# Performance work log

Hardware: AMD Instinct MI355X
Metric: run time of the kernel (lower is better)

Reference implementation:

```python
import jax, jax.numpy as jnp
import numpy as np

N = 50000    # total nodes in a batched graph
E = 200000   # directed edges (before self loops)
G = 256      # molecules per batch
F_IN = 64    # atom features
H = 4        # gat heads
CH = 128     # hidden_channels (per head)
D = H * CH   # 512, concat width
MLP_H = 128  # hidden_channels * mlp_hidden_factor
NEG_SLOPE = 0.2


def _gat(x, src, dst, W, a_src, a_dst, b, concat):
    """PyG GATConv (eval mode, self loops already added to src/dst)."""
    n = x.shape[0]
    heads, ch = a_src.shape
    h = (x @ W).reshape(n, heads, ch)                       # [N,H,C]
    e = jax.nn.leaky_relu((h * a_src).sum(-1)[src]
                          + (h * a_dst).sum(-1)[dst], NEG_SLOPE)  # [E,H]
    emax = jax.ops.segment_max(e, dst, num_segments=n)
    emax = jnp.where(jnp.isfinite(emax), emax, 0.0)
    p = jnp.exp(e - emax[dst])
    denom = jax.ops.segment_sum(p, dst, num_segments=n)
    alpha = p / (denom[dst] + 1e-16)                        # segment softmax over dst
    out = jax.ops.segment_sum(h[src] * alpha[..., None], dst, num_segments=n)
    out = out.reshape(n, heads * ch) if concat else out.mean(axis=1)
    return out + b


def _encoder(x, edge_index, batch, p):
    n = x.shape[0]
    loop = jnp.arange(n, dtype=edge_index.dtype)            # GATConv add_self_loops=True
    src = jnp.concatenate([edge_index[0], loop])
    dst = jnp.concatenate([edge_index[1], loop])
    x = jax.nn.elu(_gat(x, src, dst, p['W1'], p['as1'], p['ad1'], p['b1'], True))
    x = jax.nn.elu(_gat(x, src, dst, p['W2'], p['as2'], p['ad2'], p['b2'], True))
    x = _gat(x, src, dst, p['W3'], p['as3'], p['ad3'], p['b3'], False)
    emb = jax.ops.segment_max(x, batch, num_segments=G)     # global_max_pool
    return jnp.where(jnp.isfinite(emb), emb, 0.0)


def setup_inputs() -> dict:
    key = jax.random.key(0)
    ks = jax.random.split(key, 24)
    rn = lambda k, s, sc=0.1: jax.random.normal(k, s, jnp.float32) * sc
    return dict(
        x1=rn(ks[0], (N, F_IN), 1.0),
        edge_index1=jax.random.randint(ks[1], (2, E), 0, N, dtype=jnp.int32),
        batch1=jnp.sort(jax.random.randint(ks[2], (N,), 0, G, dtype=jnp.int32)),
        x2=rn(ks[3], (N, F_IN), 1.0),
        edge_index2=jax.random.randint(ks[4], (2, E), 0, N, dtype=jnp.int32),
        batch2=jnp.sort(jax.random.randint(ks[5], (N,), 0, G, dtype=jnp.int32)),
        W1=rn(ks[6], (F_IN, D)), as1=rn(ks[7], (H, CH)), ad1=rn(ks[8], (H, CH)),
        b1=jnp.zeros((D,), jnp.float32),
        W2=rn(ks[9], (D, D)), as2=rn(ks[10], (H, CH)), ad2=rn(ks[11], (H, CH)),
        b2=jnp.zeros((D,), jnp.float32),
        W3=rn(ks[12], (D, CH)), as3=rn(ks[13], (1, CH)), ad3=rn(ks[14], (1, CH)),
        b3=jnp.zeros((CH,), jnp.float32),
        mw1=rn(ks[15], (2 * CH, MLP_H)), mb1=jnp.zeros((MLP_H,), jnp.float32),
        mw2=rn(ks[16], (MLP_H, 1)), mb2=jnp.zeros((1,), jnp.float32),
    )


def reference(x1, edge_index1, batch1, x2, edge_index2, batch2,
              W1, as1, ad1, b1, W2, as2, ad2, b2, W3, as3, ad3, b3,
              mw1, mb1, mw2, mb2):
    p = dict(W1=W1, as1=as1, ad1=ad1, b1=b1,
             W2=W2, as2=as2, ad2=ad2, b2=b2,
             W3=W3, as3=as3, ad3=ad3, b3=b3)
    e1 = _encoder(x1, edge_index1, batch1, p)               # [G, CH]
    e2 = _encoder(x2, edge_index2, batch2, p)               # [G, CH]
    z = jnp.concatenate([e1, e2], axis=-1)                  # [G, 2*CH]
    return jax.nn.relu(z @ mw1 + mb1) @ mw2 + mb2           # [G, 1]
```

## Files before the change

### kernel.cpp

```cpp
#include <hip/hip_runtime.h>
#include <cstdint>

namespace {
constexpr int kN = 50000;
constexpr int kE = 200000;
constexpr int kE2 = kE + kN;
constexpr int kG = 256;
constexpr float kNegSlope = 0.2f;
}

using half8   = __attribute__((ext_vector_type(8))) _Float16;
using half2v  = __attribute__((ext_vector_type(2))) _Float16;
using floatx4 = __attribute__((ext_vector_type(4))) float;

__device__ __forceinline__ void gld_lds16(const void* g, void* l) {
  __builtin_amdgcn_global_load_lds(
      (const __attribute__((address_space(1))) unsigned int*)g,
      (__attribute__((address_space(3))) unsigned int*)l, 16, 0, 0);
}

__device__ __forceinline__ float fexp(float x) {
  return __builtin_amdgcn_exp2f(x * 1.44269504088896f);
}

template <int OUTF16, int BN, int CT>
__global__ __launch_bounds__(256, 2) void gemm_ring(
    const _Float16* __restrict__ A, const _Float16* __restrict__ B,
    void* __restrict__ Cv, int M, int N, int K) {
  constexpr int ASL = 512;
  constexpr int BSL = BN * 4;
  constexpr int SLOT = (ASL + BSL) * 16;
  constexpr int LPT = (ASL + BSL) / 256;
  constexpr int WTM = 64;
  constexpr int WTN = BN / 2;
  constexpr int MI = WTM / 16;
  constexpr int NI = WTN / 16;
  __shared__ alignas(16) char smem[3 * SLOT];
  const int t = threadIdx.x;
  const int w = t >> 6, l = t & 63;
  const int x = blockIdx.x & 7, s = blockIdx.x >> 3;
  const int col = (CT == 1) ? 0 : (s & (CT - 1));
  const int rt = ((CT == 1) ? s : (s >> 1)) * 8 + x;
  const int bm = rt * 128;
  const int bn = col * BN;
  if (bm >= M) return;
  const int wr = w >> 1, wc = w & 1;
  const int quad = l >> 4, lrow = l & 15;

  floatx4 acc[MI][NI];
#pragma unroll
  for (int mi = 0; mi < MI; ++mi)
#pragma unroll
    for (int ni = 0; ni < NI; ++ni) acc[mi][ni] = (floatx4){0.f, 0.f, 0.f, 0.f};

  auto stageA = [&](int slot, int kt) {
    char* buf = smem + (size_t)slot * SLOT;
    int k0 = kt * 32;
    k0 = (k0 > K - 32) ? (K - 32) : k0;
#pragma unroll
    for (int i = 0; i < ASL / 256; ++i) {
      const int sl = i * 256 + t;
      const int row = ((sl >> 6) << 4) + (sl & 15);
      const int q = (sl >> 4) & 3;
      int ga = bm + row;
      ga = (ga < M) ? ga : (M - 1);
      gld_lds16(A + (size_t)ga * K + k0 + q * 8, buf + sl * 16);
    }
  };
  auto stageB = [&](int slot, int kt) {
    char* buf = smem + (size_t)slot * SLOT + ASL * 16;
    int k0 = kt * 32;
    k0 = (k0 > K - 32) ? (K - 32) : k0;
#pragma unroll
    for (int i = 0; i < BSL / 256; ++i) {
      const int sl = i * 256 + t;
      const int row = ((sl >> 6) << 4) + (sl & 15);
      const int q = (sl >> 4) & 3;
      gld_lds16(B + (size_t)(bn + row) * K + k0 + q * 8, buf + sl * 16);
    }
  };

  stageA(0, 0); stageB(0, 0);
  stageA(1, 1); stageB(1, 1);

  const int NT = K >> 5;
  int cur = 0;
  for (int kt = 0; kt < NT; ++kt) {
    char* bufc = smem + (size_t)cur * SLOT;
    const int stg = (cur == 0) ? 2 : (cur - 1);
    if constexpr (LPT == 6)
      asm volatile("s_waitcnt vmcnt(6)" ::: "memory");
    else
      asm volatile("s_waitcnt vmcnt(4)" ::: "memory");
    __builtin_amdgcn_s_barrier();
    asm volatile("" ::: "memory");
    stageA(stg, kt + 2);
    half8 fa[MI], fb[NI];
#pragma unroll
    for (int ni = 0; ni < NI; ++ni)
      fb[ni] = *(const half8*)(bufc + ASL * 16 + ((wc * NI + ni) << 10) + l * 16);
#pragma unroll
    for (int mi = 0; mi < MI / 2; ++mi)
      fa[mi] = *(const half8*)(bufc + ((wr * MI + mi) << 10) + l * 16);
    __builtin_amdgcn_s_setprio(1);
#pragma unroll
    for (int mi = 0; mi < MI / 2; ++mi)
#pragma unroll
      for (int ni = 0; ni < NI; ++ni)
        acc[mi][ni] = __builtin_amdgcn_mfma_f32_16x16x32_f16(
            fa[mi], fb[ni], acc[mi][ni], 0, 0, 0);
    __builtin_amdgcn_s_setprio(0);
    stageB(stg, kt + 2);
#pragma unroll
    for (int mi = MI / 2; mi < MI; ++mi)
      fa[mi] = *(const half8*)(bufc + ((wr * MI + mi) << 10) + l * 16);
    __builtin_amdgcn_s_setprio(1);
#pragma unroll
    for (int mi = MI / 2; mi < MI; ++mi)
#pragma unroll
      for (int ni = 0; ni < NI; ++ni)
        acc[mi][ni] = __builtin_amdgcn_mfma_f32_16x16x32_f16(
            fa[mi], fb[ni], acc[mi][ni], 0, 0, 0);
    __builtin_amdgcn_s_setprio(0);
    cur = (cur == 2) ? 0 : (cur + 1);
  }
  asm volatile("s_waitcnt vmcnt(0)" ::: "memory");
  const int colbase = bn + wc * WTN + lrow;
#pragma unroll
  for (int mi = 0; mi < MI; ++mi) {
    const int rbase = bm + wr * WTM + mi * 16 + quad * 4;
#pragma unroll
    for (int r = 0; r < 4; ++r) {
      const int grow = rbase + r;
      if (grow < M) {
        if constexpr (OUTF16) {
          _Float16* C = (_Float16*)Cv;
#pragma unroll
          for (int ni = 0; ni < NI; ++ni)
            C[(size_t)grow * N + colbase + ni * 16] = (_Float16)acc[mi][ni][r];
        } else {
          float* C = (float*)Cv;
#pragma unroll
          for (int ni = 0; ni < NI; ++ni)
            C[(size_t)grow * N + colbase + ni * 16] = acc[mi][ni][r];
        }
      }
    }
  }
}

__global__ void wt_split_all(const float* __restrict__ W1, _Float16* Th1,
                             const float* __restrict__ W2, _Float16* Th2,
                             const float* __restrict__ W3, _Float16* Th3) {
  int idx = blockIdx.x * blockDim.x + threadIdx.x;
  const float* W;
  _Float16* Th;
  int K, N;
  if (idx < 64 * 512) {
    W = W1; Th = Th1; K = 64; N = 512;
  } else if (idx < 64 * 512 + 512 * 512) {
    idx -= 64 * 512;
    W = W2; Th = Th2; K = 512; N = 512;
  } else if (idx < 64 * 512 + 512 * 512 + 512 * 128) {
    idx -= 64 * 512 + 512 * 512;
    W = W3; Th = Th3; K = 512; N = 128;
  } else {
    return;
  }
  const int k = idx / N;
  const int n = idx - k * N;
  Th[n * K + k] = (_Float16)W[idx];
}

__global__ void prep_all(const float* __restrict__ x0, const float* __restrict__ x1,
                         _Float16* __restrict__ Xh, int* __restrict__ cnt,
                         int* __restrict__ total,
                         const float* __restrict__ W1, _Float16* Th1,
                         const float* __restrict__ W2, _Float16* Th2,
                         const float* __restrict__ W3, _Float16* Th3) {
  const int idx = blockIdx.x * blockDim.x + threadIdx.x;
  const int half = kN * 64;
  if (idx < half) {
    Xh[idx] = (_Float16)x0[idx];
  } else if (idx < 2 * half) {
    Xh[idx] = (_Float16)x1[idx - half];
  } else {
    int e = idx - 2 * half;
    const float* W;
    _Float16* Th;
    int K, N;
    if (e < 64 * 512) {
      W = W1; Th = Th1; K = 64; N = 512;
    } else if (e < 64 * 512 + 512 * 512) {
      e -= 64 * 512;
      W = W2; Th = Th2; K = 512; N = 512;
    } else if (e < 64 * 512 + 512 * 512 + 512 * 128) {
      e -= 64 * 512 + 512 * 512;
      W = W3; Th = Th3; K = 512; N = 128;
    } else {
      W = nullptr; Th = nullptr; K = N = 0;
    }
    if (W) {
      const int k = e / N;
      const int n = e - k * N;
      Th[n * K + k] = (_Float16)W[e];
    }
  }
  if (idx < 2 * kN) cnt[idx] = 1;
  if (idx == 0) *total = 0;
}
__global__ void prep(const float* __restrict__ X, _Float16* __restrict__ Xh,
                     int* __restrict__ cnt, int* __restrict__ total, int nsplit,
                     int n) {
  const int idx = blockIdx.x * blockDim.x + threadIdx.x;
  if (idx < nsplit) Xh[idx] = (_Float16)X[idx];
  if (idx < n) cnt[idx] = 1;
  if (idx == 0) *total = 0;
}

__global__ void count_edges2(const int* __restrict__ d0, const int* __restrict__ d1,
                             int* __restrict__ cnt) {
  const int i = blockIdx.x * blockDim.x + threadIdx.x;
  if (i < kE) atomicAdd(&cnt[d0[i]], 1);
  else if (i < 2 * kE) atomicAdd(&cnt[d1[i - kE] + kN], 1);
}
__global__ void fill_edges2(const int* __restrict__ s0, const int* __restrict__ d0,
                            const int* __restrict__ s1, const int* __restrict__ d1,
                            int* __restrict__ cursor, int* __restrict__ csr) {
  const int i = blockIdx.x * blockDim.x + threadIdx.x;
  if (i < kE) {
    const int p = atomicAdd(&cursor[d0[i]], 1);
    csr[p] = s0[i];
  } else if (i < 2 * kE) {
    const int j = i - kE;
    const int p = atomicAdd(&cursor[d1[j] + kN], 1);
    csr[p] = s1[j] + kN;
  }
}
__global__ void count_edges(const int* __restrict__ dst, int* __restrict__ cnt,
                            int ne) {
  const int i = blockIdx.x * blockDim.x + threadIdx.x;
  if (i < ne) atomicAdd(&cnt[dst[i]], 1);
}
__global__ void fill_edges(const int* __restrict__ src, const int* __restrict__ dst,
                           int* __restrict__ cursor, int* __restrict__ csr, int ne) {
  const int i = blockIdx.x * blockDim.x + threadIdx.x;
  if (i < ne) {
    const int p = atomicAdd(&cursor[dst[i]], 1);
    csr[p] = src[i];
  }
}
__global__ void alloc_ranges(const int* __restrict__ cnt, int* __restrict__ start,
                             int* __restrict__ cursor, int* __restrict__ total,
                             int* __restrict__ csr, int n) {
  const int i = blockIdx.x * blockDim.x + threadIdx.x;
  const int lane = threadIdx.x & 63;
  const int v = (i < n) ? cnt[i] : 0;
  int sc = v;
#pragma unroll
  for (int off = 1; off < 64; off <<= 1) {
    const int t = __shfl_up(sc, off);
    if (lane >= off) sc += t;
  }
  const int wtot = __shfl(sc, 63);
  int base = 0;
  if (lane == 63) base = atomicAdd(total, wtot);
  base = __shfl(base, 63);
  const int st = base + sc - v;
  if (i < n) {
    start[i] = st;
    cursor[i] = st + 1;
    csr[st] = i;
  }
}

__global__ void gat_agg4(const _Float16* __restrict__ h,
                         const float* __restrict__ a_src,
                         const float* __restrict__ a_dst,
                         const int* __restrict__ start, const int* __restrict__ cnt,
                         const int* __restrict__ csr_src,
                         const float* __restrict__ bias,
                         _Float16* __restrict__ outH, int n_nodes) {
  const int gtid = blockIdx.x * blockDim.x + threadIdx.x;
  const int wid = gtid >> 6;
  const int lane = threadIdx.x & 63;
  const int n0 = wid * 2;
  if (n0 >= n_nodes) return;
  const int n1r = (n0 + 1 < n_nodes) ? (n0 + 1) : n0;
  const bool has1 = (n0 + 1 < n_nodes);
  const int ch = lane * 8;
  float as_r[8], ad_r[8];
#pragma unroll
  for (int j = 0; j < 8; ++j) {
    as_r[j] = a_src[ch + j];
    ad_r[j] = a_dst[ch + j];
  }
  const int s0 = start[n0], c0 = cnt[n0];
  const int s1 = start[n1r];
  const int c1 = has1 ? cnt[n1r] : 0;
  const half8 vsA = *(const half8*)(h + (size_t)n0 * 512 + ch);
  const half8 vsB = *(const half8*)(h + (size_t)n1r * 512 + ch);
  float fsA[8], fsB[8];
  float tAs = 0.f, tAd = 0.f, tBs = 0.f, tBd = 0.f;
#pragma unroll
  for (int j = 0; j < 8; ++j) {
    fsA[j] = (float)vsA[j];
    fsB[j] = (float)vsB[j];
    tAs = fmaf(fsA[j], as_r[j], tAs);
    tAd = fmaf(fsA[j], ad_r[j], tAd);
    tBs = fmaf(fsB[j], as_r[j], tBs);
    tBd = fmaf(fsB[j], ad_r[j], tBd);
  }
#pragma unroll
  for (int off = 1; off < 16; off <<= 1) {
    tAs += __shfl_xor(tAs, off);
    tAd += __shfl_xor(tAd, off);
    tBs += __shfl_xor(tBs, off);
    tBd += __shfl_xor(tBd, off);
  }
  const float adA = tAd, adB = tBd;
  float eA = tAs + adA, eB = tBs + adB;
  eA = (eA > 0.f) ? eA : kNegSlope * eA;
  eB = (eB > 0.f) ? eB : kNegSlope * eB;
  const float wsA = fexp(eA);
  const float wsB = fexp(eB);
  float dA = wsA, dB = wsB;
  float aA[8], aB[8];
#pragma unroll
  for (int j = 0; j < 8; ++j) {
    aA[j] = wsA * fsA[j];
    aB[j] = wsB * fsB[j];
  }
  const int cm = (c0 > c1) ? c0 : c1;
  int i = 1;
  for (; i + 2 <= cm; i += 2) {
    const int jA0 = (i < c0) ? i : 0, jA1 = (i + 1 < c0) ? i + 1 : 0;
    const int jB0 = (i < c1) ? i : 0, jB1 = (i + 1 < c1) ? i + 1 : 0;
    const int sA0 = csr_src[s0 + jA0];
    const int sA1 = csr_src[s0 + jA1];
    const int sB0 = csr_src[s1 + jB0];
    const int sB1 = csr_src[s1 + jB1];
    const half8 vA0 = *(const half8*)(h + (size_t)sA0 * 512 + ch);
    const half8 vA1 = *(const half8*)(h + (size_t)sA1 * 512 + ch);
    const half8 vB0 = *(const half8*)(h + (size_t)sB0 * 512 + ch);
    const half8 vB1 = *(const half8*)(h + (size_t)sB1 * 512 + ch);
    float fA0[8], fA1[8], fB0[8], fB1[8];
    float tA0 = 0.f, tA1 = 0.f, tB0 = 0.f, tB1 = 0.f;
#pragma unroll
    for (int j = 0; j < 8; ++j) {
      fA0[j] = (float)vA0[j]; tA0 = fmaf(fA0[j], as_r[j], tA0);
      fA1[j] = (float)vA1[j]; tA1 = fmaf(fA1[j], as_r[j], tA1);
      fB0[j] = (float)vB0[j]; tB0 = fmaf(fB0[j], as_r[j], tB0);
      fB1[j] = (float)vB1[j]; tB1 = fmaf(fB1[j], as_r[j], tB1);
    }
#pragma unroll
    for (int off = 1; off < 16; off <<= 1) {
      tA0 += __shfl_xor(tA0, off);
      tA1 += __shfl_xor(tA1, off);
      tB0 += __shfl_xor(tB0, off);
      tB1 += __shfl_xor(tB1, off);
    }
    float eA0 = tA0 + adA, eA1 = tA1 + adA;
    float eB0 = tB0 + adB, eB1 = tB1 + adB;
    eA0 = (eA0 > 0.f) ? eA0 : kNegSlope * eA0;
    eA1 = (eA1 > 0.f) ? eA1 : kNegSlope * eA1;
    eB0 = (eB0 > 0.f) ? eB0 : kNegSlope * eB0;
    eB1 = (eB1 > 0.f) ? eB1 : kNegSlope * eB1;
    const float wA0 = (i < c0) ? fexp(eA0) : 0.f;
    const float wA1 = (i + 1 < c0) ? fexp(eA1) : 0.f;
    const float wB0 = (i < c1) ? fexp(eB0) : 0.f;
    const float wB1 = (i + 1 < c1) ? fexp(eB1) : 0.f;
    dA += wA0 + wA1;
    dB += wB0 + wB1;
#pragma unroll
    for (int j = 0; j < 8; ++j) {
      aA[j] = fmaf(wA0, fA0[j], aA[j]);
      aA[j] = fmaf(wA1, fA1[j], aA[j]);
      aB[j] = fmaf(wB0, fB0[j], aB[j]);
      aB[j] = fmaf(wB1, fB1[j], aB[j]);
    }
  }
  if (i < cm) {
    const int jA = (i < c0) ? i : 0;
    const int jB = (i < c1) ? i : 0;
    const int sA = csr_src[s0 + jA];
    const int sB = csr_src[s1 + jB];
    const half8 vA = *(const half8*)(h + (size_t)sA * 512 + ch);
    const half8 vB = *(const half8*)(h + (size_t)sB * 512 + ch);
    float fA[8], fB[8];
    float tA = 0.f, tB = 0.f;
#pragma unroll
    for (int j = 0; j < 8; ++j) {
      fA[j] = (float)vA[j]; tA = fmaf(fA[j], as_r[j], tA);
      fB[j] = (float)vB[j]; tB = fmaf(fB[j], as_r[j], tB);
    }
#pragma unroll
    for (int off = 1; off < 16; off <<= 1) {
      tA += __shfl_xor(tA, off);
      tB += __shfl_xor(tB, off);
    }
    float eA2 = tA + adA, eB2 = tB + adB;
    eA2 = (eA2 > 0.f) ? eA2 : kNegSlope * eA2;
    eB2 = (eB2 > 0.f) ? eB2 : kNegSlope * eB2;
    const float wA = (i < c0) ? fexp(eA2) : 0.f;
    const float wB = (i < c1) ? fexp(eB2) : 0.f;
    dA += wA;
    dB += wB;
#pragma unroll
    for (int j = 0; j < 8; ++j) {
      aA[j] = fmaf(wA, fA[j], aA[j]);
      aB[j] = fmaf(wB, fB[j], aB[j]);
    }
  }
  const float invA = 1.f / (dA + 1e-16f);
  const float invB = 1.f / (dB + 1e-16f);
  half8 HA, HB;
#pragma unroll
  for (int j = 0; j < 8; ++j) {
    float vA = aA[j] * invA + bias[ch + j];
    vA = (vA > 0.f) ? vA : (fexp(vA) - 1.f);
    HA[j] = (_Float16)vA;
    float vB = aB[j] * invB + bias[ch + j];
    vB = (vB > 0.f) ? vB : (fexp(vB) - 1.f);
    HB[j] = (_Float16)vB;
  }
  *(half8*)(outH + (size_t)n0 * 512 + ch) = HA;
  if (has1) *(half8*)(outH + (size_t)n1r * 512 + ch) = HB;
}

__global__ void gat_agg_l3(const _Float16* __restrict__ h,
                           const float* __restrict__ a_src,
                           const float* __restrict__ a_dst,
                           const int* __restrict__ start, const int* __restrict__ cnt,
                           const int* __restrict__ csr_src,
                           const float* __restrict__ bias,
                           float* __restrict__ out, int n_nodes) {
  const int gtid = blockIdx.x * blockDim.x + threadIdx.x;
  const int wid = gtid >> 6;
  const int lane = threadIdx.x & 63;
  const int n0 = wid * 2;
  if (n0 >= n_nodes) return;
  const int n1r = (n0 + 1 < n_nodes) ? (n0 + 1) : n0;
  const bool has1 = (n0 + 1 < n_nodes);
  const float2 asv = *(const float2*)(a_src + lane * 2);
  const float2 adv = *(const float2*)(a_dst + lane * 2);
  const int s0 = start[n0], c0 = cnt[n0];
  const int s1 = start[n1r];
  const int c1 = has1 ? cnt[n1r] : 0;
  const half2v vsA = *(const half2v*)(h + (size_t)n0 * 128 + lane * 2);
  const half2v vsB = *(const half2v*)(h + (size_t)n1r * 128 + lane * 2);
  const float xA = (float)vsA[0], yA = (float)vsA[1];
  const float xB = (float)vsB[0], yB = (float)vsB[1];
  float tAs = fmaf(xA, asv.x, yA * asv.y);
  float tAd = fmaf(xA, adv.x, yA * adv.y);
  float tBs = fmaf(xB, asv.x, yB * asv.y);
  float tBd = fmaf(xB, adv.x, yB * adv.y);
#pragma unroll
  for (int off = 1; off < 64; off <<= 1) {
    tAs += __shfl_xor(tAs, off);
    tAd += __shfl_xor(tAd, off);
    tBs += __shfl_xor(tBs, off);
    tBd += __shfl_xor(tBd, off);
  }
  const float adA = tAd, adB = tBd;
  float eA = tAs + adA, eB = tBs + adB;
  eA = (eA > 0.f) ? eA : kNegSlope * eA;
  eB = (eB > 0.f) ? eB : kNegSlope * eB;
  const float wsA = fexp(eA);
  const float wsB = fexp(eB);
  float dA = wsA, dB = wsB;
  float2 aA = make_float2(wsA * xA, wsA * yA);
  float2 aB = make_float2(wsB * xB, wsB * yB);
  const int cm = (c0 > c1) ? c0 : c1;
  int i = 1;
  for (; i + 2 <= cm; i += 2) {
    const int jA0 = (i < c0) ? i : 0, jA1 = (i + 1 < c0) ? i + 1 : 0;
    const int jB0 = (i < c1) ? i : 0, jB1 = (i + 1 < c1) ? i + 1 : 0;
    const int sA0 = csr_src[s0 + jA0];
    const int sA1 = csr_src[s0 + jA1];
    const int sB0 = csr_src[s1 + jB0];
    const int sB1 = csr_src[s1 + jB1];
    const half2v vA0 = *(const half2v*)(h + (size_t)sA0 * 128 + lane * 2);
    const half2v vA1 = *(const half2v*)(h + (size_t)sA1 * 128 + lane * 2);
    const half2v vB0 = *(const half2v*)(h + (size_t)sB0 * 128 + lane * 2);
    const half2v vB1 = *(const half2v*)(h + (size_t)sB1 * 128 + lane * 2);
    const float xA0 = (float)vA0[0], yA0 = (float)vA0[1];
    const float xA1 = (float)vA1[0], yA1 = (float)vA1[1];
    const float xB0 = (float)vB0[0], yB0 = (float)vB0[1];
    const float xB1 = (float)vB1[0], yB1 = (float)vB1[1];
    float tA0 = fmaf(xA0, asv.x, yA0 * asv.y);
    float tA1 = fmaf(xA1, asv.x, yA1 * asv.y);
    float tB0 = fmaf(xB0, asv.x, yB0 * asv.y);
    float tB1 = fmaf(xB1, asv.x, yB1 * asv.y);
#pragma unroll
    for (int off = 1; off < 64; off <<= 1) {
      tA0 += __shfl_xor(tA0, off);
      tA1 += __shfl_xor(tA1, off);
      tB0 += __shfl_xor(tB0, off);
      tB1 += __shfl_xor(tB1, off);
    }
    float eA0 = tA0 + adA, eA1 = tA1 + adA;
    float eB0 = tB0 + adB, eB1 = tB1 + adB;
    eA0 = (eA0 > 0.f) ? eA0 : kNegSlope * eA0;
    eA1 = (eA1 > 0.f) ? eA1 : kNegSlope * eA1;
    eB0 = (eB0 > 0.f) ? eB0 : kNegSlope * eB0;
    eB1 = (eB1 > 0.f) ? eB1 : kNegSlope * eB1;
    const float wA0 = (i < c0) ? fexp(eA0) : 0.f;
    const float wA1 = (i + 1 < c0) ? fexp(eA1) : 0.f;
    const float wB0 = (i < c1) ? fexp(eB0) : 0.f;
    const float wB1 = (i + 1 < c1) ? fexp(eB1) : 0.f;
    dA += wA0 + wA1;
    dB += wB0 + wB1;
    aA.x = fmaf(wA0, xA0, aA.x); aA.x = fmaf(wA1, xA1, aA.x);
    aA.y = fmaf(wA0, yA0, aA.y); aA.y = fmaf(wA1, yA1, aA.y);
    aB.x = fmaf(wB0, xB0, aB.x); aB.x = fmaf(wB1, xB1, aB.x);
    aB.y = fmaf(wB0, yB0, aB.y); aB.y = fmaf(wB1, yB1, aB.y);
  }
  if (i < cm) {
    const int jA = (i < c0) ? i : 0;
    const int jB = (i < c1) ? i : 0;
    const int sA = csr_src[s0 + jA];
    const int sB = csr_src[s1 + jB];
    const half2v vA = *(const half2v*)(h + (size_t)sA * 128 + lane * 2);
    const half2v vB = *(const half2v*)(h + (size_t)sB * 128 + lane * 2);
    const float xA2 = (float)vA[0], yA2 = (float)vA[1];
    const float xB2 = (float)vB[0], yB2 = (float)vB[1];
    float tA = fmaf(xA2, asv.x, yA2 * asv.y);
    float tB = fmaf(xB2, asv.x, yB2 * asv.y);
#pragma unroll
    for (int off = 1; off < 64; off <<= 1) {
      tA += __shfl_xor(tA, off);
      tB += __shfl_xor(tB, off);
    }
    float eA2 = tA + adA, eB2 = tB + adB;
    eA2 = (eA2 > 0.f) ? eA2 : kNegSlope * eA2;
    eB2 = (eB2 > 0.f) ? eB2 : kNegSlope * eB2;
    const float wA = (i < c0) ? fexp(eA2) : 0.f;
    const float wB = (i < c1) ? fexp(eB2) : 0.f;
    dA += wA;
    dB += wB;
    aA.x = fmaf(wA, xA2, aA.x);
    aA.y = fmaf(wA, yA2, aA.y);
    aB.x = fmaf(wB, xB2, aB.x);
    aB.y = fmaf(wB, yB2, aB.y);
  }
  const float invA = 1.f / (dA + 1e-16f);
  const float invB = 1.f / (dB + 1e-16f);
  *(float2*)(out + (size_t)n0 * 128 + lane * 2) =
      make_float2(aA.x * invA + bias[lane * 2],
                  aA.y * invA + bias[lane * 2 + 1]);
  if (has1)
    *(float2*)(out + (size_t)n1r * 128 + lane * 2) =
        make_float2(aB.x * invB + bias[lane * 2],
                    aB.y * invB + bias[lane * 2 + 1]);
}

__global__ void pool_max2(const float* __restrict__ x, const int* __restrict__ bt1,
                          const int* __restrict__ bt2, float* __restrict__ emb) {
  __shared__ int lohi[2];
  const int enc = blockIdx.x >> 8;
  const int g = blockIdx.x & 255;
  const int* batch = enc ? bt2 : bt1;
  const float* xx = x + (size_t)enc * kN * 128;
  if (threadIdx.x == 0) {
    int lo = 0, hi = kN;
    while (lo < hi) {
      const int mid = (lo + hi) >> 1;
      if (batch[mid] < g) lo = mid + 1; else hi = mid;
    }
    lohi[0] = lo;
    hi = kN;
    while (lo < hi) {
      const int mid = (lo + hi) >> 1;
      if (batch[mid] < g + 1) lo = mid + 1; else hi = mid;
    }
    lohi[1] = lo;
  }
  __syncthreads();
  const int lo = lohi[0], hi = lohi[1];
  const int c = threadIdx.x;
  float m = -1e30f;
  for (int nid = lo; nid < hi; ++nid) m = fmaxf(m, xx[(size_t)nid * 128 + c]);
  emb[(size_t)blockIdx.x * 128 + c] = (lo < hi) ? m : 0.f;
}
__global__ void pool_max(const float* __restrict__ x, const int* __restrict__ batch,
                         float* __restrict__ emb, int n_nodes) {
  __shared__ int lohi[2];
  const int g = blockIdx.x;
  if (threadIdx.x == 0) {
    int lo = 0, hi = n_nodes;
    while (lo < hi) {
      const int mid = (lo + hi) >> 1;
      if (batch[mid] < g) lo = mid + 1; else hi = mid;
    }
    lohi[0] = lo;
    hi = n_nodes;
    while (lo < hi) {
      const int mid = (lo + hi) >> 1;
      if (batch[mid] < g + 1) lo = mid + 1; else hi = mid;
    }
    lohi[1] = lo;
  }
  __syncthreads();
  const int lo = lohi[0], hi = lohi[1];
  const int c = threadIdx.x;
  float m = -1e30f;
  for (int nid = lo; nid < hi; ++nid) m = fmaxf(m, x[(size_t)nid * 128 + c]);
  emb[g * 128 + c] = (lo < hi) ? m : 0.f;
}

__global__ void mlp_head(const float* __restrict__ e1, const float* __restrict__ e2,
                         const float* __restrict__ mw1, const float* __restrict__ mb1,
                         const float* __restrict__ mw2, const float* __restrict__ mb2,
                         float* __restrict__ out) {
  __shared__ float z[256];
  __shared__ float red[128];
  const int g = blockIdx.x;
  const int j = threadIdx.x;
  z[j] = e1[g * 128 + j];
  z[j + 128] = e2[g * 128 + j];
  __syncthreads();
  float acc = mb1[j];
  for (int k = 0; k < 256; ++k) acc = fmaf(z[k], mw1[k * 128 + j], acc);
  acc = fmaxf(acc, 0.f) * mw2[j];
  red[j] = acc;
  __syncthreads();
  for (int s = 64; s > 0; s >>= 1) {
    if (j < s) red[j] += red[j + s];
    __syncthreads();
  }
  if (j == 0) out[g] = red[0] + mb2[0];
}

namespace {
struct Bufs {
  _Float16 *R1h, *R2h;
  float *R1f, *R2f, *asrc, *adst;
  int *cnt, *start, *cursor, *csr, *total;
  _Float16 *Wth1, *Wth2, *Wth3;
  float* emb;
  size_t need;
};

Bufs plan(void* d_ws, int M, int E) {
  Bufs b;
  char* w = (char*)d_ws;
  size_t off = 0;
  auto take = [&](size_t bytes) -> void* {
    void* p = w + off;
    off += (bytes + 255) & ~(size_t)255;
    return p;
  };
  b.R1h = (_Float16*)take((size_t)M * 512 * 2);
  b.R1f = (float*)b.R1h;
  b.R2h = (_Float16*)take((size_t)M * 512 * 2);
  b.R2f = (float*)b.R2h;
  b.asrc = (float*)take((size_t)M * 4 * 4);
  b.adst = (float*)take((size_t)M * 4 * 4);
  b.cnt = (int*)take((size_t)M * 4);
  b.start = (int*)take((size_t)M * 4);
  b.cursor = (int*)take((size_t)M * 4);
  b.csr = (int*)take((size_t)E * 4);
  b.total = (int*)take(256);
  b.Wth1 = (_Float16*)take((size_t)64 * 512 * 2);
  b.Wth2 = (_Float16*)take((size_t)512 * 512 * 2);
  b.Wth3 = (_Float16*)take((size_t)512 * 128 * 2);
  b.emb = (float*)take((size_t)2 * kG * 128 * 4);
  b.need = off;
  return b;
}

void run_layers(const Bufs& b, void* const* d_in, int M, hipStream_t stream) {
  const float* as1 = (const float*)d_in[7];
  const float* ad1 = (const float*)d_in[8];
  const float* b1 = (const float*)d_in[9];
  const float* as2 = (const float*)d_in[11];
  const float* ad2 = (const float*)d_in[12];
  const float* b2 = (const float*)d_in[13];
  const float* as3 = (const float*)d_in[15];
  const float* ad3 = (const float*)d_in[16];
  const float* b3 = (const float*)d_in[17];
  const int aggBlocks = (((M + 1) / 2) * 64 + 255) / 256;
  const int RT = (M + 127) / 128;
  const int SP = (RT + 7) / 8;

  gemm_ring<1, 256, 2><<<SP * 16, 256, 0, stream>>>(b.R1h, b.Wth1, b.R2h, M, 512, 64);
  gat_agg4<<<aggBlocks, 256, 0, stream>>>(b.R2h, as1, ad1, b.start, b.cnt,
                                          b.csr, b1, b.R1h, M);
  gemm_ring<1, 256, 2><<<SP * 16, 256, 0, stream>>>(b.R1h, b.Wth2, b.R2h, M, 512, 512);
  gat_agg4<<<aggBlocks, 256, 0, stream>>>(b.R2h, as2, ad2, b.start, b.cnt,
                                          b.csr, b2, b.R1h, M);
  gemm_ring<1, 128, 1><<<SP * 8, 256, 0, stream>>>(b.R1h, b.Wth3, b.R2h, M, 128, 512);
  gat_agg_l3<<<aggBlocks, 256, 0, stream>>>(b.R2h, as3, ad3, b.start, b.cnt,
                                            b.csr, b3, b.R1f, M);
}
}

extern "C" void kernel_launch(void* const* d_in, const int* in_sizes, int n_in,
                              void* d_out, int out_size, void* d_ws, size_t ws_size,
                              hipStream_t stream) {
  (void)in_sizes; (void)n_in; (void)out_size;
  const float* W1 = (const float*)d_in[6];
  const float* W2 = (const float*)d_in[10];
  const float* W3 = (const float*)d_in[14];
  const float* mw1 = (const float*)d_in[18];
  const float* mb1 = (const float*)d_in[19];
  const float* mw2 = (const float*)d_in[20];
  const float* mb2 = (const float*)d_in[21];

  Bufs bc = plan(d_ws, 2 * kN, 2 * kE2);
  const bool combined = bc.need <= ws_size;
  Bufs b = combined ? bc : plan(d_ws, kN, kE2);

  const int wtot = 64 * 512 + 512 * 512 + 512 * 128;
  if (combined) {
    const int M = 2 * kN;
    const int* ei0 = (const int*)d_in[1];
    const int* ei1 = (const int*)d_in[4];
    prep_all<<<(M * 64 + wtot + 255) / 256, 256, 0, stream>>>(
        (const float*)d_in[0], (const float*)d_in[3], b.R1h, b.cnt, b.total,
        W1, b.Wth1, W2, b.Wth2, W3, b.Wth3);
    count_edges2<<<(2 * kE + 255) / 256, 256, 0, stream>>>(ei0 + kE, ei1 + kE,
                                                           b.cnt);
    alloc_ranges<<<(M + 255) / 256, 256, 0, stream>>>(b.cnt, b.start, b.cursor,
                                                      b.total, b.csr, M);
    fill_edges2<<<(2 * kE + 255) / 256, 256, 0, stream>>>(ei0, ei0 + kE, ei1,
                                                          ei1 + kE, b.cursor, b.csr);
    run_layers(b, d_in, M, stream);
    pool_max2<<<2 * kG, 128, 0, stream>>>(b.R1f, (const int*)d_in[2],
                                          (const int*)d_in[5], b.emb);
  } else {
    wt_split_all<<<(wtot + 255) / 256, 256, 0, stream>>>(W1, b.Wth1, W2, b.Wth2,
                                                         W3, b.Wth3);
    for (int enc = 0; enc < 2; ++enc) {
      const float* x = (const float*)d_in[enc * 3 + 0];
      const int* ei = (const int*)d_in[enc * 3 + 1];
      const int* batch = (const int*)d_in[enc * 3 + 2];
      prep<<<(kN * 64 + 255) / 256, 256, 0, stream>>>(x, b.R1h, b.cnt, b.total,
                                                      kN * 64, kN);
      count_edges<<<(kE + 255) / 256, 256, 0, stream>>>(ei + kE, b.cnt, kE);
      alloc_ranges<<<(kN + 255) / 256, 256, 0, stream>>>(b.cnt, b.start, b.cursor,
                                                         b.total, b.csr, kN);
      fill_edges<<<(kE + 255) / 256, 256, 0, stream>>>(ei, ei + kE, b.cursor, b.csr,
                                                       kE);
      run_layers(b, d_in, kN, stream);
      pool_max<<<kG, 128, 0, stream>>>(b.R1f, batch, b.emb + (size_t)enc * kG * 128,
                                       kN);
    }
  }
  mlp_head<<<kG, 128, 0, stream>>>(b.emb, b.emb + (size_t)kG * 128, mw1, mb1, mw2,
                                   mb2, (float*)d_out);
}
```

Before: 633.2 us.

## Use 256x256 tiles with 512 threads and a 4-deep ring for layer-2 GEMM

```diff
diff --git a/kernel.cpp b/kernel.cpp
--- a/kernel.cpp
+++ b/kernel.cpp
@@ -23,28 +23,35 @@
   return __builtin_amdgcn_exp2f(x * 1.44269504088896f);
 }
 
-template <int OUTF16, int BN, int CT>
-__global__ __launch_bounds__(256, 2) void gemm_ring(
+template <int OUTF16, int BM, int BN, int CT>
+__global__ __launch_bounds__((BM == 256) ? 512 : 256, 2) void gemm_ring(
     const _Float16* __restrict__ A, const _Float16* __restrict__ B,
     void* __restrict__ Cv, int M, int N, int K) {
-  constexpr int ASL = 512;
+  constexpr int THREADS = (BM == 256) ? 512 : 256;
+  constexpr int ASL = BM * 4;
   constexpr int BSL = BN * 4;
   constexpr int SLOT = (ASL + BSL) * 16;
-  constexpr int LPT = (ASL + BSL) / 256;
-  constexpr int WTM = 64;
-  constexpr int WTN = BN / 2;
+  constexpr int LPT = (ASL + BSL) / THREADS;
+  constexpr int RING = (BM == 256) ? 4 : 3;
+  constexpr int DIST = RING - 1;
+  constexpr int WAITN = (DIST - 1) * LPT;
+  constexpr int WAVES = THREADS / 64;
+  constexpr int WN = (BM == 256) ? 4 : 2;
+  constexpr int WM = WAVES / WN;
+  constexpr int WTM = BM / WM;
+  constexpr int WTN = BN / WN;
   constexpr int MI = WTM / 16;
   constexpr int NI = WTN / 16;
-  __shared__ alignas(16) char smem[3 * SLOT];
+  __shared__ alignas(16) char smem[RING * SLOT];
   const int t = threadIdx.x;
   const int w = t >> 6, l = t & 63;
   const int x = blockIdx.x & 7, s = blockIdx.x >> 3;
   const int col = (CT == 1) ? 0 : (s & (CT - 1));
   const int rt = ((CT == 1) ? s : (s >> 1)) * 8 + x;
-  const int bm = rt * 128;
+  const int bm = rt * BM;
   const int bn = col * BN;
   if (bm >= M) return;
-  const int wr = w >> 1, wc = w & 1;
+  const int wr = w / WN, wc = w % WN;
   const int quad = l >> 4, lrow = l & 15;
 
   floatx4 acc[MI][NI];
@@ -58,8 +65,8 @@
     int k0 = kt * 32;
     k0 = (k0 > K - 32) ? (K - 32) : k0;
 #pragma unroll
-    for (int i = 0; i < ASL / 256; ++i) {
-      const int sl = i * 256 + t;
+    for (int i = 0; i < ASL / THREADS; ++i) {
+      const int sl = i * THREADS + t;
       const int row = ((sl >> 6) << 4) + (sl & 15);
       const int q = (sl >> 4) & 3;
       int ga = bm + row;
@@ -72,29 +79,34 @@
     int k0 = kt * 32;
     k0 = (k0 > K - 32) ? (K - 32) : k0;
 #pragma unroll
-    for (int i = 0; i < BSL / 256; ++i) {
-      const int sl = i * 256 + t;
+    for (int i = 0; i < BSL / THREADS; ++i) {
+      const int sl = i * THREADS + t;
       const int row = ((sl >> 6) << 4) + (sl & 15);
       const int q = (sl >> 4) & 3;
       gld_lds16(B + (size_t)(bn + row) * K + k0 + q * 8, buf + sl * 16);
     }
   };
 
-  stageA(0, 0); stageB(0, 0);
-  stageA(1, 1); stageB(1, 1);
+#pragma unroll
+  for (int p = 0; p < DIST; ++p) {
+    stageA(p, p);
+    stageB(p, p);
+  }
 
   const int NT = K >> 5;
   int cur = 0;
   for (int kt = 0; kt < NT; ++kt) {
     char* bufc = smem + (size_t)cur * SLOT;
-    const int stg = (cur == 0) ? 2 : (cur - 1);
-    if constexpr (LPT == 6)
+    const int stg = (cur == 0) ? (RING - 1) : (cur - 1);
+    if constexpr (WAITN == 8)
+      asm volatile("s_waitcnt vmcnt(8)" ::: "memory");
+    else if constexpr (WAITN == 6)
       asm volatile("s_waitcnt vmcnt(6)" ::: "memory");
     else
       asm volatile("s_waitcnt vmcnt(4)" ::: "memory");
     __builtin_amdgcn_s_barrier();
     asm volatile("" ::: "memory");
-    stageA(stg, kt + 2);
+    stageA(stg, kt + DIST);
     half8 fa[MI], fb[NI];
 #pragma unroll
     for (int ni = 0; ni < NI; ++ni)
@@ -110,7 +122,7 @@
         acc[mi][ni] = __builtin_amdgcn_mfma_f32_16x16x32_f16(
             fa[mi], fb[ni], acc[mi][ni], 0, 0, 0);
     __builtin_amdgcn_s_setprio(0);
-    stageB(stg, kt + 2);
+    stageB(stg, kt + DIST);
 #pragma unroll
     for (int mi = MI / 2; mi < MI; ++mi)
       fa[mi] = *(const half8*)(bufc + ((wr * MI + mi) << 10) + l * 16);
@@ -122,7 +134,7 @@
         acc[mi][ni] = __builtin_amdgcn_mfma_f32_16x16x32_f16(
             fa[mi], fb[ni], acc[mi][ni], 0, 0, 0);
     __builtin_amdgcn_s_setprio(0);
-    cur = (cur == 2) ? 0 : (cur + 1);
+    cur = (cur == RING - 1) ? 0 : (cur + 1);
   }
   asm volatile("s_waitcnt vmcnt(0)" ::: "memory");
   const int colbase = bn + wc * WTN + lrow;
@@ -681,16 +693,21 @@
   const float* ad3 = (const float*)d_in[16];
   const float* b3 = (const float*)d_in[17];
   const int aggBlocks = (((M + 1) / 2) * 64 + 255) / 256;
-  const int RT = (M + 127) / 128;
-  const int SP = (RT + 7) / 8;
-
-  gemm_ring<1, 256, 2><<<SP * 16, 256, 0, stream>>>(b.R1h, b.Wth1, b.R2h, M, 512, 64);
+  const int RT128 = (M + 127) / 128;
+  const int SP128 = (RT128 + 7) / 8;
+  const int RT256 = (M + 255) / 256;
+  const int SP256 = (RT256 + 7) / 8;
+
+  gemm_ring<1, 128, 256, 2><<<SP128 * 16, 256, 0, stream>>>(b.R1h, b.Wth1, b.R2h,
+                                                            M, 512, 64);
   gat_agg4<<<aggBlocks, 256, 0, stream>>>(b.R2h, as1, ad1, b.start, b.cnt,
                                           b.csr, b1, b.R1h, M);
-  gemm_ring<1, 256, 2><<<SP * 16, 256, 0, stream>>>(b.R1h, b.Wth2, b.R2h, M, 512, 512);
+  gemm_ring<1, 256, 256, 2><<<SP256 * 16, 512, 0, stream>>>(b.R1h, b.Wth2, b.R2h,
+                                                            M, 512, 512);
   gat_agg4<<<aggBlocks, 256, 0, stream>>>(b.R2h, as2, ad2, b.start, b.cnt,
                                           b.csr, b2, b.R1h, M);
-  gemm_ring<1, 128, 1><<<SP * 8, 256, 0, stream>>>(b.R1h, b.Wth3, b.R2h, M, 128, 512);
+  gemm_ring<1, 128, 128, 1><<<SP128 * 8, 256, 0, stream>>>(b.R1h, b.Wth3, b.R2h,
+                                                           M, 128, 512);
   gat_agg_l3<<<aggBlocks, 256, 0, stream>>>(b.R2h, as3, ad3, b.start, b.cnt,
                                             b.csr, b3, b.R1f, M);
 }
```

Result: no change. 633.4 us (+0.0%).
